# Optimization experiments

Measured on AMD Instinct MI355X. Metric: run time of the kernel, lower is better.

## Reference

```python
import jax, jax.numpy as jnp
import numpy as np

N_NODES = 100000
N_EDGES = 3200000
NEG_SLOPE = 0.2  # PyG GATConv default
EPS = 1e-16      # PyG softmax denominator guard


def setup_inputs() -> dict:
    key = jax.random.key(0)
    ks = jax.random.split(key, 12)
    x = jax.random.normal(ks[0], (N_NODES, 4), dtype=jnp.float32)
    edge_index = jax.random.randint(ks[1], (2, N_EDGES), 0, N_NODES, dtype=jnp.int32)
    # conv1: in=4, heads=4, out=16, concat -> 64
    W1 = jax.random.normal(ks[2], (4, 64), dtype=jnp.float32) * 0.5
    a_src1 = jax.random.normal(ks[3], (4, 16), dtype=jnp.float32) * 0.3
    a_dst1 = jax.random.normal(ks[4], (4, 16), dtype=jnp.float32) * 0.3
    b1 = jnp.zeros((64,), dtype=jnp.float32)
    # conv2: in=64, heads=1, out=2, no concat
    W2 = jax.random.normal(ks[5], (64, 2), dtype=jnp.float32) * 0.2
    a_src2 = jax.random.normal(ks[6], (1, 2), dtype=jnp.float32) * 0.3
    a_dst2 = jax.random.normal(ks[7], (1, 2), dtype=jnp.float32) * 0.3
    b2 = jnp.zeros((2,), dtype=jnp.float32)
    return dict(x=x, edge_index=edge_index, W1=W1, a_src1=a_src1, a_dst1=a_dst1,
                b1=b1, W2=W2, a_src2=a_src2, a_dst2=a_dst2, b2=b2)


def _gat_layer(h_in, src, dst, W, a_s, a_d, b, heads, out_dim, concat):
    n = h_in.shape[0]
    h = (h_in @ W).reshape(n, heads, out_dim)            # [N, H, F]
    alpha_s = jnp.einsum('nhf,hf->nh', h, a_s)           # [N, H]
    alpha_d = jnp.einsum('nhf,hf->nh', h, a_d)
    e = jax.nn.leaky_relu(alpha_s[src] + alpha_d[dst], NEG_SLOPE)  # [E, H]
    # segment softmax over incoming edges of each dst node
    m = jax.ops.segment_max(e, dst, num_segments=n)      # [N, H]
    e = jnp.exp(e - m[dst])
    s = jax.ops.segment_sum(e, dst, num_segments=n)
    alpha = e / (s[dst] + EPS)                            # [E, H]
    msg = h[src] * alpha[:, :, None]                      # [E, H, F]
    out = jax.ops.segment_sum(msg, dst, num_segments=n)   # [N, H, F]
    if concat:
        out = out.reshape(n, heads * out_dim)
    else:
        out = out.mean(axis=1)
    return out + b


def reference(x, edge_index, W1, a_src1, a_dst1, b1, W2, a_src2, a_dst2, b2):
    n = x.shape[0]
    loop = jnp.arange(n, dtype=edge_index.dtype)
    src = jnp.concatenate([edge_index[0], loop])  # PyG add_self_loops=True
    dst = jnp.concatenate([edge_index[1], loop])
    h = jax.nn.elu(_gat_layer(x, src, dst, W1, a_src1, a_dst1, b1, 4, 16, True))
    h = _gat_layer(h, src, dst, W2, a_src2, a_dst2, b2, 1, 2, False)
    return jax.nn.log_softmax(h, axis=1)
```

## Files before the change

### kernel.cpp

```cpp
#include <hip/hip_runtime.h>
#include <hip/hip_fp16.h>
#include <math.h>

#define NEG_SLOPE 0.2f
#define EPS_F 1e-16f

#define P1_NB 256
#define P1S_THREADS 1024
#define LOCAL_BITS 7
#define NLOCAL 128
#define MAX_BEDGES 5632
#define SCAN_SHIFT 11

__device__ __forceinline__ float leaky(float v) {
    return v >= 0.f ? v : NEG_SLOPE * v;
}

__global__ void k_phaseA(const float* __restrict__ x, const float* __restrict__ W1,
                         const float* __restrict__ a_src1, const float* __restrict__ a_dst1,
                         __half* __restrict__ h1h, float* __restrict__ as1,
                         float* __restrict__ ad1, int N) {
    int node = blockIdx.x * 4 + (threadIdx.x >> 6);
    if (node >= N) return;
    int lane = threadIdx.x & 63;
    float x0 = x[node * 4 + 0], x1 = x[node * 4 + 1];
    float x2 = x[node * 4 + 2], x3 = x[node * 4 + 3];
    float h = x0 * W1[lane] + x1 * W1[64 + lane] + x2 * W1[128 + lane] + x3 * W1[192 + lane];
    h1h[(size_t)node * 64 + lane] = __float2half(h);
    float as = h * a_src1[lane];
    float ad = h * a_dst1[lane];
#pragma unroll
    for (int m = 8; m >= 1; m >>= 1) {
        as += __shfl_xor(as, m, 16);
        ad += __shfl_xor(ad, m, 16);
    }
    if ((lane & 15) == 0) {
        int head = lane >> 4;
        as1[node * 4 + head] = as;
        ad1[node * 4 + head] = ad;
    }
}

__global__ void k_p1hist(const int* __restrict__ dst, int* __restrict__ histT,
                         int E, int chunk, int nbucket) {
    __shared__ int cnt[1024];
    int blk = blockIdx.x, t = threadIdx.x;
    for (int i = t; i < nbucket; i += P1S_THREADS) cnt[i] = 0;
    __syncthreads();
    int s = blk * chunk, e = min(E, s + chunk);
    for (int i = s + t; i < e; i += P1S_THREADS)
        atomicAdd(&cnt[dst[i] >> LOCAL_BITS], 1);
    __syncthreads();
    for (int i = t; i < nbucket; i += P1S_THREADS)
        histT[i * P1_NB + blk] = cnt[i];
}

__global__ void k_scan1(const int* __restrict__ in, int* __restrict__ out,
                        int* __restrict__ blockSums, int M) {
    __shared__ int sdata[256];
    int t = threadIdx.x;
    int base = blockIdx.x * 2048 + t * 8;
    int v[8];
    int total = 0;
#pragma unroll
    for (int k = 0; k < 8; ++k) {
        int idx = base + k;
        v[k] = (idx < M) ? in[idx] : 0;
        total += v[k];
    }
    sdata[t] = total;
    __syncthreads();
    for (int off = 1; off < 256; off <<= 1) {
        int x = (t >= off) ? sdata[t - off] : 0;
        __syncthreads();
        sdata[t] += x;
        __syncthreads();
    }
    int run = sdata[t] - total;
#pragma unroll
    for (int k = 0; k < 8; ++k) {
        int idx = base + k;
        if (idx < M) out[idx] = run;
        run += v[k];
    }
    if (t == 255) blockSums[blockIdx.x] = sdata[255];
}

__global__ void k_scan2(int* __restrict__ bs, int n) {
    __shared__ int s[128];
    int t = threadIdx.x;
    int v = (t < n) ? bs[t] : 0;
    s[t] = v;
    __syncthreads();
    for (int o = 1; o < 128; o <<= 1) {
        int x = (t >= o) ? s[t - o] : 0;
        __syncthreads();
        s[t] += x;
        __syncthreads();
    }
    if (t < n) bs[t] = s[t] - v;
}

__global__ void k_p1scatter(const int* __restrict__ src, const int* __restrict__ dst,
                            const int* __restrict__ baseT, const int* __restrict__ bsScan,
                            unsigned int* __restrict__ packed,
                            int E, int chunk, int nbucket) {
    __shared__ int cnt[1024];
    int blk = blockIdx.x, t = threadIdx.x;
    for (int i = t; i < nbucket; i += P1S_THREADS) {
        int idx = i * P1_NB + blk;
        cnt[i] = baseT[idx] + bsScan[idx >> SCAN_SHIFT];
    }
    __syncthreads();
    int s = blk * chunk, e = min(E, s + chunk);
    for (int i = s + t; i < e; i += P1S_THREADS) {
        int d = dst[i];
        int pos = atomicAdd(&cnt[d >> LOCAL_BITS], 1);
        packed[pos] = ((unsigned int)(d & (NLOCAL - 1)) << 23) | (unsigned int)src[i];
    }
}

__global__ void __launch_bounds__(1024, 8)
k_fineL1(const unsigned int* __restrict__ packed, const int* __restrict__ baseT,
         const int* __restrict__ bsScan,
         const __half* __restrict__ h1h, const float* __restrict__ as1,
         const float* __restrict__ ad1, const float* __restrict__ b1,
         const float* __restrict__ W2, const float* __restrict__ a_src2,
         const float* __restrict__ a_dst2,
         int* __restrict__ csr, int* __restrict__ rowptr,
         uint2* __restrict__ node2, int N, int E) {
    __shared__ int cnt[NLOCAL];
    __shared__ int off[NLOCAL];
    __shared__ int cur[NLOCAL];
    __shared__ unsigned int eb[MAX_BEDGES];

    int b = blockIdx.x, t = threadIdx.x;
    int nbucket = gridDim.x;

    int i0 = b * P1_NB;
    int startE = baseT[i0] + bsScan[i0 >> SCAN_SHIFT];
    int endE = E;
    if (b != nbucket - 1) {
        int i1 = (b + 1) * P1_NB;
        endE = baseT[i1] + bsScan[i1 >> SCAN_SHIFT];
    }
    int ne = endE - startE;
    if (ne > MAX_BEDGES) ne = MAX_BEDGES;

    if (t < NLOCAL) cnt[t] = 0;
    __syncthreads();
    for (int i = t; i < ne; i += 1024)
        atomicAdd(&cnt[packed[startE + i] >> 23], 1);
    __syncthreads();
    if (t < NLOCAL) cur[t] = cnt[t];
    __syncthreads();
    for (int o = 1; o < NLOCAL; o <<= 1) {
        int v = (t < NLOCAL && t >= o) ? cur[t - o] : 0;
        __syncthreads();
        if (t < NLOCAL) cur[t] += v;
        __syncthreads();
    }
    if (t < NLOCAL) {
        int excl = cur[t] - cnt[t];
        off[t] = excl;
        int node = (b << LOCAL_BITS) + t;
        if (node < N) rowptr[node] = startE + excl;
    }
    if (b == 0 && t == 0) rowptr[N] = E;
    __syncthreads();
    if (t < NLOCAL) cur[t] = off[t];
    __syncthreads();
    for (int i = t; i < ne; i += 1024) {
        unsigned int p = packed[startE + i];
        int pos = atomicAdd(&cur[p >> 23], 1);
        eb[pos] = p;
    }
    __syncthreads();
    for (int i = t; i < ne; i += 1024)
        csr[startE + i] = (int)(eb[i] & 0x7FFFFFu);

    int wave = t >> 6;
    int lane = t & 63;
    int sub  = lane >> 4;
    int fl   = lane & 15;
    int h    = fl >> 2;
    bool pacc = ((fl & 3) == 0);
    int nodeBase = b << LOCAL_BITS;

    for (int q = 0; q < 8; ++q) {
        int local = wave * 8 + q;
        int node = nodeBase + local;
        if (node >= N) break;
        int beg = off[local];
        int end = beg + cnt[local];

        float ad_h = ad1[node * 4 + h];
        float ps_h = __expf(leaky(as1[node * 4 + h] + ad_h));

        float psum = (pacc && sub == 0) ? ps_h : 0.f;
        float a0 = 0.f, a1 = 0.f, a2 = 0.f, a3 = 0.f;
        if (sub == 0) {
            float2 raw = *(const float2*)(h1h + ((size_t)node << 6) + (fl << 2));
            __half2 h01 = *reinterpret_cast<__half2*>(&raw.x);
            __half2 h23 = *reinterpret_cast<__half2*>(&raw.y);
            float2 f01 = __half22float2(h01), f23 = __half22float2(h23);
            a0 = ps_h * f01.x; a1 = ps_h * f01.y;
            a2 = ps_h * f23.x; a3 = ps_h * f23.y;
        }

        for (int c = beg; c < end; c += 16) {
#pragma unroll
            for (int m = 0; m < 4; ++m) {
                int e = c + m * 4 + sub;
                bool valid = e < end;
                int s = (int)(eb[valid ? e : beg] & 0x7FFFFFu);
                float v = leaky(as1[s * 4 + h] + ad_h);
                float p = valid ? __expf(v) : 0.f;
                if (pacc) psum += p;
                float2 raw = *(const float2*)(h1h + ((size_t)s << 6) + (fl << 2));
                __half2 h01 = *reinterpret_cast<__half2*>(&raw.x);
                __half2 h23 = *reinterpret_cast<__half2*>(&raw.y);
                float2 f01 = __half22float2(h01), f23 = __half22float2(h23);
                a0 = fmaf(p, f01.x, a0);
                a1 = fmaf(p, f01.y, a1);
                a2 = fmaf(p, f23.x, a2);
                a3 = fmaf(p, f23.y, a3);
            }
        }

        a0 += __shfl_xor(a0, 16); a0 += __shfl_xor(a0, 32);
        a1 += __shfl_xor(a1, 16); a1 += __shfl_xor(a1, 32);
        a2 += __shfl_xor(a2, 16); a2 += __shfl_xor(a2, 32);
        a3 += __shfl_xor(a3, 16); a3 += __shfl_xor(a3, 32);

        psum += __shfl_xor(psum, 16); psum += __shfl_xor(psum, 32);
        float psumF = __shfl(psum, h << 2);
        float inv = 1.f / (psumF + EPS_F);

        float4 b1v = ((const float4*)b1)[fl];
        float o0 = a0 * inv + b1v.x;
        float o1 = a1 * inv + b1v.y;
        float o2 = a2 * inv + b1v.z;
        float o3 = a3 * inv + b1v.w;
        float e0 = o0 > 0.f ? o0 : (__expf(o0) - 1.f);
        float e1 = o1 > 0.f ? o1 : (__expf(o1) - 1.f);
        float e2 = o2 > 0.f ? o2 : (__expf(o2) - 1.f);
        float e3 = o3 > 0.f ? o3 : (__expf(o3) - 1.f);

        float4 w01 = ((const float4*)W2)[fl * 2];
        float4 w23 = ((const float4*)W2)[fl * 2 + 1];
        float c0 = e0 * w01.x + e1 * w01.z + e2 * w23.x + e3 * w23.z;
        float c1 = e0 * w01.y + e1 * w01.w + e2 * w23.y + e3 * w23.w;
#pragma unroll
        for (int m = 8; m >= 1; m >>= 1) {
            c0 += __shfl_xor(c0, m);
            c1 += __shfl_xor(c1, m);
        }
        if (lane == 0) {
            float as2 = c0 * a_src2[0] + c1 * a_src2[1];
            float ad2 = c0 * a_dst2[0] + c1 * a_dst2[1];
            __half2 hc = __floats2half2_rn(c0, c1);
            __half2 ha = __floats2half2_rn(as2, ad2);
            node2[node] = make_uint2(*(unsigned int*)&hc, *(unsigned int*)&ha);
        }
    }
}

__global__ void k_layer2(const int* __restrict__ rowptr, const int* __restrict__ csr,
                         const uint2* __restrict__ node2, const float* __restrict__ b2,
                         float* __restrict__ out, int N) {
    int node = blockIdx.x * 16 + (threadIdx.x >> 4);
    if (node >= N) return;
    int sl = threadIdx.x & 15;

    uint2 mraw = node2[node];
    __half2 mch = *reinterpret_cast<__half2*>(&mraw.x);
    __half2 mah = *reinterpret_cast<__half2*>(&mraw.y);
    float2 mc = __half22float2(mch);
    float2 ma = __half22float2(mah);
    float ad = ma.y;
    int beg = rowptr[node], end = rowptr[node + 1];

    float psum = 0.f, a0 = 0.f, a1 = 0.f;
    for (int e = beg + sl; e < end; e += 16) {
        uint2 sraw = node2[csr[e]];
        __half2 sch = *reinterpret_cast<__half2*>(&sraw.x);
        __half2 sah = *reinterpret_cast<__half2*>(&sraw.y);
        float2 sc = __half22float2(sch);
        float2 sa = __half22float2(sah);
        float p = __expf(leaky(sa.x + ad));
        psum += p;
        a0 = fmaf(p, sc.x, a0);
        a1 = fmaf(p, sc.y, a1);
    }
    if (sl == 0) {
        float p = __expf(leaky(ma.x + ad));
        psum += p;
        a0 = fmaf(p, mc.x, a0);
        a1 = fmaf(p, mc.y, a1);
    }
#pragma unroll
    for (int m = 8; m >= 1; m >>= 1) {
        psum += __shfl_xor(psum, m);
        a0 += __shfl_xor(a0, m);
        a1 += __shfl_xor(a1, m);
    }
    if (sl == 0) {
        float inv = 1.f / (psum + EPS_F);
        float o0 = a0 * inv + b2[0];
        float o1 = a1 * inv + b2[1];
        float mx = fmaxf(o0, o1);
        float lse = mx + logf(__expf(o0 - mx) + __expf(o1 - mx));
        out[node * 2 + 0] = o0 - lse;
        out[node * 2 + 1] = o1 - lse;
    }
}


extern "C" void kernel_launch(void* const* d_in, const int* in_sizes, int n_in,
                              void* d_out, int out_size, void* d_ws, size_t ws_size,
                              hipStream_t stream) {
    const float* x      = (const float*)d_in[0];
    const int*   ei     = (const int*)d_in[1];
    const float* W1     = (const float*)d_in[2];
    const float* a_src1 = (const float*)d_in[3];
    const float* a_dst1 = (const float*)d_in[4];
    const float* b1     = (const float*)d_in[5];
    const float* W2     = (const float*)d_in[6];
    const float* a_src2 = (const float*)d_in[7];
    const float* a_dst2 = (const float*)d_in[8];
    const float* b2     = (const float*)d_in[9];
    float* out = (float*)d_out;

    int N = in_sizes[0] / 4;
    int E = in_sizes[1] / 2;
    const int* e_src = ei;
    const int* e_dst = ei + E;

    int nbucket = (N + NLOCAL - 1) >> LOCAL_BITS;
    int M = nbucket * P1_NB;

    char* w = (char*)d_ws;
    auto alloc = [&](size_t bytes) -> void* {
        void* p = (void*)w;
        w += (bytes + 255) & ~(size_t)255;
        return p;
    };
    __half* h1h       = (__half*)alloc((size_t)N * 64 * 2);
    float*  as1       = (float*)alloc((size_t)N * 4 * 4);
    float*  ad1       = (float*)alloc((size_t)N * 4 * 4);
    uint2*  node2     = (uint2*)alloc((size_t)N * 8);
    int*    rowptr    = (int*)alloc((size_t)(N + 1) * 4);
    int*    histT     = (int*)alloc((size_t)M * 4);
    int*    baseT     = (int*)alloc((size_t)M * 4);
    int*    blockSums = (int*)alloc(256 * 4);
    int*    csr       = (int*)alloc((size_t)E * 4);
    unsigned int* packed = (unsigned int*)alloc((size_t)E * 4);

    int chunk = (E + P1_NB - 1) / P1_NB;
    int nbScan = (M + 2047) / 2048;
    int nodeb = (N + 3) / 4;

    k_phaseA<<<nodeb, 256, 0, stream>>>(x, W1, a_src1, a_dst1, h1h, as1, ad1, N);
    k_p1hist<<<P1_NB, P1S_THREADS, 0, stream>>>(e_dst, histT, E, chunk, nbucket);
    k_scan1<<<nbScan, 256, 0, stream>>>(histT, baseT, blockSums, M);
    k_scan2<<<1, 128, 0, stream>>>(blockSums, nbScan);
    k_p1scatter<<<P1_NB, P1S_THREADS, 0, stream>>>(e_src, e_dst, baseT, blockSums,
                                                   packed, E, chunk, nbucket);
    k_fineL1<<<nbucket, 1024, 0, stream>>>(packed, baseT, blockSums,
                                           h1h, as1, ad1, b1, W2,
                                           a_src2, a_dst2, csr, rowptr, node2, N, E);
    k_layer2<<<(N + 15) / 16, 256, 0, stream>>>(rowptr, csr, node2, b2, out, N);
}
```

Before: 252.4 us.

## Remap layer-1 aggregation to one wave per node, one lane per feature

Replaces the 4-edge-subgroup by 16-lane float2 mapping in the fused layer-1 aggregation with a mapping where each lane owns one of the 64 features and the whole wave walks every edge of the node, unrolled by four. This removes the cross-subgroup shuffle reductions and the padded-edge masking. The cost is redundant exp and as1 loads per lane and 2-byte gathers per edge instead of 8-byte ones. The bucket-sort pass also keeps the packed edges in registers between the counting and scatter passes instead of reading global memory twice, and leaky ReLU now uses fmaxf.

```diff
diff --git a/kernel.cpp b/kernel.cpp
--- a/kernel.cpp
+++ b/kernel.cpp
@@ -10,10 +10,11 @@
 #define LOCAL_BITS 7
 #define NLOCAL 128
 #define MAX_BEDGES 5632
+#define REGS_PB 6
 #define SCAN_SHIFT 11
 
 __device__ __forceinline__ float leaky(float v) {
-    return v >= 0.f ? v : NEG_SLOPE * v;
+    return fmaxf(v, NEG_SLOPE * v);
 }
 
 __global__ void k_phaseA(const float* __restrict__ x, const float* __restrict__ W1,
@@ -149,8 +150,16 @@
 
     if (t < NLOCAL) cnt[t] = 0;
     __syncthreads();
-    for (int i = t; i < ne; i += 1024)
-        atomicAdd(&cnt[packed[startE + i] >> 23], 1);
+
+    unsigned int pk[REGS_PB];
+#pragma unroll
+    for (int k = 0; k < REGS_PB; ++k) {
+        int i = t + k * 1024;
+        pk[k] = (i < ne) ? packed[startE + i] : 0xFFFFFFFFu;
+    }
+#pragma unroll
+    for (int k = 0; k < REGS_PB; ++k)
+        if (pk[k] != 0xFFFFFFFFu) atomicAdd(&cnt[pk[k] >> 23], 1);
     __syncthreads();
     if (t < NLOCAL) cur[t] = cnt[t];
     __syncthreads();
@@ -170,22 +179,23 @@
     __syncthreads();
     if (t < NLOCAL) cur[t] = off[t];
     __syncthreads();
-    for (int i = t; i < ne; i += 1024) {
-        unsigned int p = packed[startE + i];
-        int pos = atomicAdd(&cur[p >> 23], 1);
-        eb[pos] = p;
-    }
+#pragma unroll
+    for (int k = 0; k < REGS_PB; ++k)
+        if (pk[k] != 0xFFFFFFFFu) {
+            int pos = atomicAdd(&cur[pk[k] >> 23], 1);
+            eb[pos] = pk[k];
+        }
     __syncthreads();
     for (int i = t; i < ne; i += 1024)
         csr[startE + i] = (int)(eb[i] & 0x7FFFFFu);
 
     int wave = t >> 6;
     int lane = t & 63;
-    int sub  = lane >> 4;
-    int fl   = lane & 15;
-    int h    = fl >> 2;
-    bool pacc = ((fl & 3) == 0);
+    int h = lane >> 4;
     int nodeBase = b << LOCAL_BITS;
+
+    float2 w2 = ((const float2*)W2)[lane];
+    float b1v = b1[lane];
 
     for (int q = 0; q < 8; ++q) {
         int local = wave * 8 + q;
@@ -195,64 +205,52 @@
         int end = beg + cnt[local];
 
         float ad_h = ad1[node * 4 + h];
-        float ps_h = __expf(leaky(as1[node * 4 + h] + ad_h));
-
-        float psum = (pacc && sub == 0) ? ps_h : 0.f;
-        float a0 = 0.f, a1 = 0.f, a2 = 0.f, a3 = 0.f;
-        if (sub == 0) {
-            float2 raw = *(const float2*)(h1h + ((size_t)node << 6) + (fl << 2));
-            __half2 h01 = *reinterpret_cast<__half2*>(&raw.x);
-            __half2 h23 = *reinterpret_cast<__half2*>(&raw.y);
-            float2 f01 = __half22float2(h01), f23 = __half22float2(h23);
-            a0 = ps_h * f01.x; a1 = ps_h * f01.y;
-            a2 = ps_h * f23.x; a3 = ps_h * f23.y;
-        }
-
-        for (int c = beg; c < end; c += 16) {
-#pragma unroll
-            for (int m = 0; m < 4; ++m) {
-                int e = c + m * 4 + sub;
-                bool valid = e < end;
-                int s = (int)(eb[valid ? e : beg] & 0x7FFFFFu);
-                float v = leaky(as1[s * 4 + h] + ad_h);
-                float p = valid ? __expf(v) : 0.f;
-                if (pacc) psum += p;
-                float2 raw = *(const float2*)(h1h + ((size_t)s << 6) + (fl << 2));
-                __half2 h01 = *reinterpret_cast<__half2*>(&raw.x);
-                __half2 h23 = *reinterpret_cast<__half2*>(&raw.y);
-                float2 f01 = __half22float2(h01), f23 = __half22float2(h23);
-                a0 = fmaf(p, f01.x, a0);
-                a1 = fmaf(p, f01.y, a1);
-                a2 = fmaf(p, f23.x, a2);
-                a3 = fmaf(p, f23.y, a3);
-            }
-        }
-
-        a0 += __shfl_xor(a0, 16); a0 += __shfl_xor(a0, 32);
-        a1 += __shfl_xor(a1, 16); a1 += __shfl_xor(a1, 32);
-        a2 += __shfl_xor(a2, 16); a2 += __shfl_xor(a2, 32);
-        a3 += __shfl_xor(a3, 16); a3 += __shfl_xor(a3, 32);
-
-        psum += __shfl_xor(psum, 16); psum += __shfl_xor(psum, 32);
-        float psumF = __shfl(psum, h << 2);
-        float inv = 1.f / (psumF + EPS_F);
-
-        float4 b1v = ((const float4*)b1)[fl];
-        float o0 = a0 * inv + b1v.x;
-        float o1 = a1 * inv + b1v.y;
-        float o2 = a2 * inv + b1v.z;
-        float o3 = a3 * inv + b1v.w;
-        float e0 = o0 > 0.f ? o0 : (__expf(o0) - 1.f);
-        float e1 = o1 > 0.f ? o1 : (__expf(o1) - 1.f);
-        float e2 = o2 > 0.f ? o2 : (__expf(o2) - 1.f);
-        float e3 = o3 > 0.f ? o3 : (__expf(o3) - 1.f);
-
-        float4 w01 = ((const float4*)W2)[fl * 2];
-        float4 w23 = ((const float4*)W2)[fl * 2 + 1];
-        float c0 = e0 * w01.x + e1 * w01.z + e2 * w23.x + e3 * w23.z;
-        float c1 = e0 * w01.y + e1 * w01.w + e2 * w23.y + e3 * w23.w;
-#pragma unroll
-        for (int m = 8; m >= 1; m >>= 1) {
+        float ps = __expf(leaky(as1[node * 4 + h] + ad_h));
+        float hself = __half2float(h1h[((size_t)node << 6) + lane]);
+        float acc = ps * hself;
+        float psum = ps;
+
+        int c = beg;
+        for (; c + 4 <= end; c += 4) {
+            int s0 = (int)(eb[c + 0] & 0x7FFFFFu);
+            int s1 = (int)(eb[c + 1] & 0x7FFFFFu);
+            int s2 = (int)(eb[c + 2] & 0x7FFFFFu);
+            int s3 = (int)(eb[c + 3] & 0x7FFFFFu);
+            float v0 = as1[s0 * 4 + h] + ad_h;
+            float v1 = as1[s1 * 4 + h] + ad_h;
+            float v2 = as1[s2 * 4 + h] + ad_h;
+            float v3 = as1[s3 * 4 + h] + ad_h;
+            float hh0 = __half2float(h1h[((size_t)s0 << 6) + lane]);
+            float hh1 = __half2float(h1h[((size_t)s1 << 6) + lane]);
+            float hh2 = __half2float(h1h[((size_t)s2 << 6) + lane]);
+            float hh3 = __half2float(h1h[((size_t)s3 << 6) + lane]);
+            float p0 = __expf(leaky(v0));
+            float p1 = __expf(leaky(v1));
+            float p2 = __expf(leaky(v2));
+            float p3 = __expf(leaky(v3));
+            psum += (p0 + p1) + (p2 + p3);
+            acc = fmaf(p0, hh0, acc);
+            acc = fmaf(p1, hh1, acc);
+            acc = fmaf(p2, hh2, acc);
+            acc = fmaf(p3, hh3, acc);
+        }
+        for (; c < end; ++c) {
+            int s = (int)(eb[c] & 0x7FFFFFu);
+            float v = as1[s * 4 + h] + ad_h;
+            float hh = __half2float(h1h[((size_t)s << 6) + lane]);
+            float p = __expf(leaky(v));
+            psum += p;
+            acc = fmaf(p, hh, acc);
+        }
+
+        float inv = 1.f / (psum + EPS_F);
+        float o = acc * inv + b1v;
+        float el = o > 0.f ? o : (__expf(o) - 1.f);
+
+        float c0 = el * w2.x;
+        float c1 = el * w2.y;
+#pragma unroll
+        for (int m = 32; m >= 1; m >>= 1) {
             c0 += __shfl_xor(c0, m);
             c1 += __shfl_xor(c1, m);
         }
```

New measurement: 285.3 us. 13.0% more time.
